# Optimization experiments

Measured on AMD Instinct MI355X. Metric: run time of the kernel, lower is better.

Reference implementation:

```python
import jax, jax.numpy as jnp
import numpy as np

B = 8192          # batch
CIN = 256         # in_channels
COUT = 64         # out_channels
K = 3             # kernel_size
NK = 4            # num_kernels
HIDDEN = int(CIN * 0.25)   # attention hidden = int(in_channels*ratio) = 64
TEMP = 34.0       # attention temperature
KAN_IN = 64 * 4   # base*4 = flattened conv output (COUT*2*2)
GRID_SIZE, SPLINE_ORDER = 5, 3
GMIN, GMAX = -1.0, 1.0
NUM_BASES = GRID_SIZE + SPLINE_ORDER  # 8


def setup_inputs() -> dict:
    key = jax.random.key(0)
    ks = jax.random.split(key, 8)
    s = 0.05
    return {
        "x": jax.random.normal(ks[0], (B, CIN, 4, 4), jnp.float32),
        # dynamic-conv kernel bank [num_kernels, out, in, k, k]
        "weight": jax.random.normal(ks[1], (NK, COUT, CIN, K, K), jnp.float32) * s,
        "bias": jnp.zeros((NK, COUT), jnp.float32),
        # Attention2D: GAP -> fc1 (1x1 conv == linear) -> ReLU -> fc2 -> softmax(/T)
        "fc1_w": jax.random.normal(ks[2], (HIDDEN, CIN), jnp.float32) * s,
        "fc1_b": jnp.zeros((HIDDEN,), jnp.float32),
        "fc2_w": jax.random.normal(ks[3], (NK, HIDDEN), jnp.float32) * s,
        "fc2_b": jnp.zeros((NK,), jnp.float32),
        # KANLinear params (efficient-KAN style)
        "kan_base_w": jax.random.normal(ks[4], (COUT, KAN_IN), jnp.float32) * s,
        "kan_spline_w": jax.random.normal(ks[5], (COUT, KAN_IN, NUM_BASES), jnp.float32) * s,
        "kan_spline_scaler": jnp.ones((COUT, KAN_IN), jnp.float32),
    }


def _bspline_bases(x):
    """Cox-de Boor B-spline bases; x [B, F] -> [B, F, GRID_SIZE+SPLINE_ORDER]."""
    h = (GMAX - GMIN) / GRID_SIZE
    # extended grid, shared across features: length grid_size + 2*order + 1 = 12
    grid = jnp.arange(-SPLINE_ORDER, GRID_SIZE + SPLINE_ORDER + 1, dtype=x.dtype) * h + GMIN
    xe = x[..., None]  # [B, F, 1]
    bases = ((xe >= grid[:-1]) & (xe < grid[1:])).astype(x.dtype)  # order 0
    for k in range(1, SPLINE_ORDER + 1):
        left = (xe - grid[: -(k + 1)]) / (grid[k:-1] - grid[: -(k + 1)]) * bases[..., :-1]
        right = (grid[k + 1:] - xe) / (grid[k + 1:] - grid[1:-k]) * bases[..., 1:]
        bases = left + right
    return bases  # [B, F, 8]


def reference(x, weight, bias, fc1_w, fc1_b, fc2_w, fc2_b,
              kan_base_w, kan_spline_w, kan_spline_scaler):
    b = x.shape[0]
    # --- Attention2D: softmax over kernel bank ---
    pooled = x.mean(axis=(2, 3))                                  # [B, CIN]
    hid = jax.nn.relu(pooled @ fc1_w.T + fc1_b)                   # [B, HIDDEN]
    attn = jax.nn.softmax((hid @ fc2_w.T + fc2_b) / TEMP, axis=-1)  # [B, NK]
    # --- per-sample dynamic conv, fused form ---
    # sum_k a[b,k] * conv(x, W_k) == conv with per-sample aggregated weight
    w_all = weight.reshape(NK * COUT, CIN, K, K)
    y = jax.lax.conv_general_dilated(
        x, w_all, window_strides=(1, 1), padding="VALID",
        dimension_numbers=("NCHW", "OIHW", "NCHW"))                # [B, NK*COUT, 2, 2]
    y = y.reshape(b, NK, COUT, y.shape[-2], y.shape[-1])
    conv_out = jnp.einsum("bk,bkohw->bohw", attn, y)
    conv_out = conv_out + (attn @ bias)[:, :, None, None]          # aggregated bias
    # --- KANLinear on flattened conv output ---
    feat = conv_out.reshape(b, -1)                                 # [B, 256]
    base_out = jax.nn.silu(feat) @ kan_base_w.T                    # [B, COUT]
    bases = _bspline_bases(feat)                                   # [B, 256, 8]
    spline_out = jnp.einsum("big,oig->bo", bases,
                            kan_spline_w * kan_spline_scaler[..., None])
    return base_out + spline_out                                   # [B, COUT]
```

## Files before the change

### kernel.cpp

```cpp
#include <hip/hip_runtime.h>

#define BT   8192
#define MS   16

typedef _Float16 half8  __attribute__((ext_vector_type(8)));
typedef _Float16 half4v __attribute__((ext_vector_type(4)));
typedef float    floatx4  __attribute__((ext_vector_type(4)));
typedef float    floatx16 __attribute__((ext_vector_type(16)));

__global__ __launch_bounds__(256) void w3_transform(
    const float* __restrict__ weight, _Float16* __restrict__ W3)
{
    const int n = blockIdx.x;
    const int c = threadIdx.x;
    const float* src = weight + ((size_t)n * 256 + c) * 9;
    const int cc = c >> 5, ci = c & 31;
    #pragma unroll
    for (int ij = 0; ij < 9; ++ij) {
        W3[((size_t)(cc * 9 + ij) * 256 + n) * 32 + ci] = (_Float16)src[ij];
    }
}

__global__ __launch_bounds__(256) void wk3_transform(
    const float* __restrict__ base_w, const float* __restrict__ spline_w,
    const float* __restrict__ scaler, const float* __restrict__ fc1_w,
    _Float16* __restrict__ Wk3, _Float16* __restrict__ Wf3)
{
    const int st = blockIdx.x;
    const int tid = threadIdx.x;
    if (st < 72) {
        #pragma unroll
        for (int u = 0; u < 8; ++u) {
            const int idx = u * 256 + tid;
            const int n = idx >> 5, kk = idx & 31;
            const int k = st * 32 + kk;
            float v;
            if (k < 256) {
                v = base_w[n * 256 + k];
            } else {
                const int r = k - 256;
                const int i = r >> 3, g = r & 7;
                v = spline_w[((size_t)n * 256 + i) * 8 + g] * scaler[n * 256 + i];
            }
            Wk3[(size_t)st * 2048 + idx] = (_Float16)v;
        }
    } else {
        const int st2 = st - 72;
        #pragma unroll
        for (int u = 0; u < 8; ++u) {
            const int idx = u * 256 + tid;
            const int n = idx >> 5, kk = idx & 31;
            Wf3[(size_t)st2 * 2048 + idx] = (_Float16)fc1_w[n * 256 + st2 * 32 + kk];
        }
    }
}

__device__ __forceinline__ void bases8(float xv, _Float16* dst) {
    float g[12];
    #pragma unroll
    for (int u = 0; u < 12; ++u) g[u] = (float)(u - 3) * 0.4f - 1.0f;
    float dt[12];
    #pragma unroll
    for (int u = 0; u < 12; ++u) dt[u] = xv - g[u];
    float t0[11];
    #pragma unroll
    for (int t = 0; t < 11; ++t)
        t0[t] = (xv >= g[t] && xv < g[t + 1]) ? 1.f : 0.f;
    float t1[10];
    #pragma unroll
    for (int t = 0; t < 10; ++t)
        t1[t] = dt[t] * (1.0f / (g[t + 1] - g[t])) * t0[t]
              - dt[t + 2] * (1.0f / (g[t + 2] - g[t + 1])) * t0[t + 1];
    float t2[9];
    #pragma unroll
    for (int t = 0; t < 9; ++t)
        t2[t] = dt[t] * (1.0f / (g[t + 2] - g[t])) * t1[t]
              - dt[t + 3] * (1.0f / (g[t + 3] - g[t + 1])) * t1[t + 1];
    half8 hb;
    #pragma unroll
    for (int t = 0; t < 8; ++t) {
        float b = dt[t] * (1.0f / (g[t + 3] - g[t])) * t2[t]
                - dt[t + 4] * (1.0f / (g[t + 4] - g[t + 1])) * t2[t + 1];
        hb[t] = (_Float16)b;
    }
    *(half8*)dst = hb;
}

__global__ __launch_bounds__(512, 4) void fused_kernel(
    const float* __restrict__ x, const _Float16* __restrict__ W3,
    const _Float16* __restrict__ Wk3, const _Float16* __restrict__ Wf3,
    const float* __restrict__ bias, const float* __restrict__ fc1_b,
    const float* __restrict__ fc2_w, const float* __restrict__ fc2_b,
    float* __restrict__ out)
{
    __shared__ __align__(16) char smem[16 * 2312 * 2];
    __shared__ float hid_lds[16 * 68];
    __shared__ float attn_s[16][4];

    _Float16* Xs  = (_Float16*)smem;
    _Float16* Pl  = (_Float16*)(smem + 20992);
    _Float16* Act = (_Float16*)smem;

    const int tid = threadIdx.x;
    const int wv = tid >> 6, lane = tid & 63;
    const int nl = lane & 15, q = lane >> 4;
    const int cg = wv & 3, rh = wv >> 2;
    const int b0 = blockIdx.x * MS;

    const int posr = nl & 3;
    const int aLane = (nl >> 2) * 656 + ((posr >> 1) * 4 + (posr & 1)) * 40 + q * 8;
    int lbW[4];
    #pragma unroll
    for (int kb = 0; kb < 4; ++kb) lbW[kb] = ((cg + 4 * kb) * 16 + nl) * 32 + q * 8;

    const int s_ = tid >> 5, cch = tid & 31;
    const float* xg = x + ((size_t)(b0 + s_) * 256 + cch) * 16;
    _Float16* xd = &Xs[s_ * 656 + cch];

    floatx4 acc[2][4];
    #pragma unroll
    for (int rr = 0; rr < 2; ++rr)
        #pragma unroll
        for (int kb = 0; kb < 4; ++kb) acc[rr][kb] = floatx4{0.f, 0.f, 0.f, 0.f};

    floatx16 r = *(const floatx16*)xg;

    for (int cc = 0; cc < 8; ++cc) {
        __syncthreads();
        #pragma unroll
        for (int p = 0; p < 16; ++p) xd[p * 40] = (_Float16)r[p];
        {
            float sm = 0.f;
            #pragma unroll
            for (int p = 0; p < 16; ++p) sm += r[p];
            Pl[s_ * 264 + cc * 32 + cch] = (_Float16)(sm * (1.0f / 16.0f));
        }
        if (cc < 7) r = *(const floatx16*)(xg + (cc + 1) * 512);
        __syncthreads();

        #pragma unroll 3
        for (int ij = 0; ij < 9; ++ij) {
            const int step = cc * 9 + ij;
            const int p0 = (ij / 3) * 4 + (ij % 3);
            const _Float16* wstep = W3 + (size_t)step * 8192;
            half8 bF[4];
            #pragma unroll
            for (int kb = 0; kb < 4; ++kb) bF[kb] = *(const half8*)(wstep + lbW[kb]);
            half8 aF[2];
            #pragma unroll
            for (int rr = 0; rr < 2; ++rr)
                aF[rr] = *(const half8*)&Xs[(rh * 2 + rr) * 2624 + aLane + p0 * 40];
            #pragma unroll
            for (int rr = 0; rr < 2; ++rr)
                #pragma unroll
                for (int kb = 0; kb < 4; ++kb)
                    acc[rr][kb] = __builtin_amdgcn_mfma_f32_16x16x32_f16(aF[rr], bF[kb], acc[rr][kb], 0, 0, 0);
        }
    }

    if (rh == 0) {
        floatx4 a1 = floatx4{0.f, 0.f, 0.f, 0.f};
        const _Float16* wfb = Wf3 + ((cg * 16 + nl) * 32 + q * 8);
        const _Float16* pb = &Pl[nl * 264 + q * 8];
        #pragma unroll
        for (int st = 0; st < 8; ++st) {
            const half8 aF = *(const half8*)(pb + st * 32);
            const half8 bF = *(const half8*)(wfb + st * 2048);
            a1 = __builtin_amdgcn_mfma_f32_16x16x32_f16(aF, bF, a1, 0, 0, 0);
        }
        const int h = cg * 16 + nl;
        const float fb = fc1_b[h];
        #pragma unroll
        for (int reg = 0; reg < 4; ++reg)
            hid_lds[(q * 4 + reg) * 68 + h] = fmaxf(a1[reg] + fb, 0.f);
    }
    __syncthreads();

    if (wv == 0) {
        const int s = lane >> 2, kb = lane & 3;
        float l = fc2_b[kb];
        #pragma unroll 8
        for (int h = 0; h < 64; ++h) l += hid_lds[s * 68 + h] * fc2_w[kb * 64 + h];
        float m = fmaxf(l, __shfl_xor(l, 1));
        m = fmaxf(m, __shfl_xor(m, 2));
        const float e = __expf((l - m) * (1.0f / 34.0f));
        float sm = e + __shfl_xor(e, 1);
        sm += __shfl_xor(sm, 2);
        attn_s[s][kb] = e / sm;
    }
    __syncthreads();

    {
        const int o = cg * 16 + nl;
        const float bb0 = bias[o], bb1 = bias[64 + o], bb2 = bias[128 + o], bb3 = bias[192 + o];
        #pragma unroll
        for (int rr = 0; rr < 2; ++rr) {
            const int s = (rh * 2 + rr) * 4 + q;
            const float a0 = attn_s[s][0], a1 = attn_s[s][1], a2 = attn_s[s][2], a3 = attn_s[s][3];
            const float badd = a0 * bb0 + a1 * bb1 + a2 * bb2 + a3 * bb3;
            float f[4];
            #pragma unroll
            for (int e = 0; e < 4; ++e)
                f[e] = a0 * acc[rr][0][e] + a1 * acc[rr][1][e]
                     + a2 * acc[rr][2][e] + a3 * acc[rr][3][e] + badd;
            half4v sv;
            #pragma unroll
            for (int e = 0; e < 4; ++e) {
                const float ex = __expf(-f[e]);
                sv[e] = (_Float16)(f[e] * __builtin_amdgcn_rcpf(1.f + ex));
            }
            *(half4v*)&Act[s * 2312 + o * 4] = sv;
            #pragma unroll
            for (int e = 0; e < 4; ++e)
                bases8(f[e], &Act[s * 2312 + 256 + (o * 4 + e) * 8]);
        }
    }
    __syncthreads();

    {
        floatx4 a2 = floatx4{0.f, 0.f, 0.f, 0.f};
        const _Float16* wkb = Wk3 + ((size_t)(cg * 16 + nl) * 32 + q * 8);
        const _Float16* ab = &Act[nl * 2312 + q * 8];
        #pragma unroll 6
        for (int i = 0; i < 36; ++i) {
            const int st = rh * 36 + i;
            const half8 aF = *(const half8*)(ab + st * 32);
            const half8 bF = *(const half8*)(wkb + (size_t)st * 2048);
            a2 = __builtin_amdgcn_mfma_f32_16x16x32_f16(aF, bF, a2, 0, 0, 0);
        }
        if (rh == 1) *(floatx4*)&hid_lds[cg * 256 + lane * 4] = a2;
        __syncthreads();
        if (rh == 0) {
            const floatx4 p = *(const floatx4*)&hid_lds[cg * 256 + lane * 4];
            a2 = a2 + p;
            #pragma unroll
            for (int reg = 0; reg < 4; ++reg)
                out[(size_t)(b0 + q * 4 + reg) * 64 + cg * 16 + nl] = a2[reg];
        }
    }
}

extern "C" void kernel_launch(void* const* d_in, const int* in_sizes, int n_in,
                              void* d_out, int out_size, void* d_ws, size_t ws_size,
                              hipStream_t stream) {
    const float* x          = (const float*)d_in[0];
    const float* weight     = (const float*)d_in[1];
    const float* bias       = (const float*)d_in[2];
    const float* fc1_w      = (const float*)d_in[3];
    const float* fc1_b      = (const float*)d_in[4];
    const float* fc2_w      = (const float*)d_in[5];
    const float* fc2_b      = (const float*)d_in[6];
    const float* kan_base_w = (const float*)d_in[7];
    const float* kan_spline = (const float*)d_in[8];
    const float* kan_scaler = (const float*)d_in[9];
    float* out = (float*)d_out;

    _Float16* W3  = (_Float16*)d_ws;
    _Float16* Wk3 = W3 + (size_t)72 * 8192;
    _Float16* Wf3 = Wk3 + (size_t)72 * 2048;

    w3_transform<<<256, 256, 0, stream>>>(weight, W3);
    wk3_transform<<<80, 256, 0, stream>>>(kan_base_w, kan_spline, kan_scaler,
                                          fc1_w, Wk3, Wf3);
    fused_kernel<<<BT / MS, 512, 0, stream>>>(x, W3, Wk3, Wf3, bias, fc1_b,
                                              fc2_w, fc2_b, out);
}
```

Measured before the change: 276.6 us.

## Shrink tile to 8 samples, double-buffer x in LDS, prefetch weight fragments

The fused kernel now handles 8 samples per block with 256 threads instead of 16 with 512, so there are twice as many blocks and each wave covers all sample rows. The x staging buffer is double-buffered so the next channel chunk is written to LDS while the current one is consumed, which removes one barrier per chunk. Weight fragments for the conv and KAN MFMAs are software-prefetched one step ahead. The trade-off is that the MFMA M dimension (16) is now only half used in the attention and KAN stages, and every block re-reads the full weight set, doubling global weight traffic per sample.

```diff
diff --git a/kernel.cpp b/kernel.cpp
--- a/kernel.cpp
+++ b/kernel.cpp
@@ -1,7 +1,8 @@
 #include <hip/hip_runtime.h>
 
 #define BT   8192
-#define MS   16
+#define MS   8
+#define XBUF (MS * 656)
 
 typedef _Float16 half8  __attribute__((ext_vector_type(8)));
 typedef _Float16 half4v __attribute__((ext_vector_type(4)));
@@ -86,25 +87,25 @@
     *(half8*)dst = hb;
 }
 
-__global__ __launch_bounds__(512, 4) void fused_kernel(
+__global__ __launch_bounds__(256, 4) void fused_kernel(
     const float* __restrict__ x, const _Float16* __restrict__ W3,
     const _Float16* __restrict__ Wk3, const _Float16* __restrict__ Wf3,
     const float* __restrict__ bias, const float* __restrict__ fc1_b,
     const float* __restrict__ fc2_w, const float* __restrict__ fc2_b,
     float* __restrict__ out)
 {
-    __shared__ __align__(16) char smem[16 * 2312 * 2];
-    __shared__ float hid_lds[16 * 68];
-    __shared__ float attn_s[16][4];
+    __shared__ __align__(16) char smem[MS * 2312 * 2];
+    __shared__ float hid_lds[MS * 68];
+    __shared__ float attn_s[MS][4];
 
     _Float16* Xs  = (_Float16*)smem;
-    _Float16* Pl  = (_Float16*)(smem + 20992);
+    _Float16* Pl  = (_Float16*)(smem + 2 * XBUF * 2);
     _Float16* Act = (_Float16*)smem;
 
     const int tid = threadIdx.x;
     const int wv = tid >> 6, lane = tid & 63;
     const int nl = lane & 15, q = lane >> 4;
-    const int cg = wv & 3, rh = wv >> 2;
+    const int cg = wv;
     const int b0 = blockIdx.x * MS;
 
     const int posr = nl & 3;
@@ -115,78 +116,101 @@
 
     const int s_ = tid >> 5, cch = tid & 31;
     const float* xg = x + ((size_t)(b0 + s_) * 256 + cch) * 16;
-    _Float16* xd = &Xs[s_ * 656 + cch];
 
     floatx4 acc[2][4];
     #pragma unroll
-    for (int rr = 0; rr < 2; ++rr)
-        #pragma unroll
-        for (int kb = 0; kb < 4; ++kb) acc[rr][kb] = floatx4{0.f, 0.f, 0.f, 0.f};
+    for (int rt = 0; rt < 2; ++rt)
+        #pragma unroll
+        for (int kb = 0; kb < 4; ++kb) acc[rt][kb] = floatx4{0.f, 0.f, 0.f, 0.f};
 
     floatx16 r = *(const floatx16*)xg;
+    {
+        _Float16* xd = &Xs[s_ * 656 + cch];
+        #pragma unroll
+        for (int p = 0; p < 16; ++p) xd[p * 40] = (_Float16)r[p];
+        float sm = 0.f;
+        #pragma unroll
+        for (int p = 0; p < 16; ++p) sm += r[p];
+        Pl[s_ * 264 + cch] = (_Float16)(sm * (1.0f / 16.0f));
+    }
+    r = *(const floatx16*)(xg + 512);
+    __syncthreads();
 
     for (int cc = 0; cc < 8; ++cc) {
-        __syncthreads();
-        #pragma unroll
-        for (int p = 0; p < 16; ++p) xd[p * 40] = (_Float16)r[p];
-        {
+        const int cur = cc & 1;
+        if (cc < 7) {
+            _Float16* xd = &Xs[(cur ^ 1) * XBUF + s_ * 656 + cch];
+            #pragma unroll
+            for (int p = 0; p < 16; ++p) xd[p * 40] = (_Float16)r[p];
             float sm = 0.f;
             #pragma unroll
             for (int p = 0; p < 16; ++p) sm += r[p];
-            Pl[s_ * 264 + cc * 32 + cch] = (_Float16)(sm * (1.0f / 16.0f));
-        }
-        if (cc < 7) r = *(const floatx16*)(xg + (cc + 1) * 512);
-        __syncthreads();
-
-        #pragma unroll 3
+            Pl[s_ * 264 + (cc + 1) * 32 + cch] = (_Float16)(sm * (1.0f / 16.0f));
+        }
+        if (cc < 6) r = *(const floatx16*)(xg + (cc + 2) * 512);
+
+        const _Float16* wst = W3 + (size_t)cc * 9 * 8192;
+        const _Float16* xb = &Xs[cur * XBUF + aLane];
+        half8 bFc[4];
+        #pragma unroll
+        for (int kb = 0; kb < 4; ++kb) bFc[kb] = *(const half8*)(wst + lbW[kb]);
+        #pragma unroll
         for (int ij = 0; ij < 9; ++ij) {
-            const int step = cc * 9 + ij;
-            const int p0 = (ij / 3) * 4 + (ij % 3);
-            const _Float16* wstep = W3 + (size_t)step * 8192;
-            half8 bF[4];
-            #pragma unroll
-            for (int kb = 0; kb < 4; ++kb) bF[kb] = *(const half8*)(wstep + lbW[kb]);
-            half8 aF[2];
-            #pragma unroll
-            for (int rr = 0; rr < 2; ++rr)
-                aF[rr] = *(const half8*)&Xs[(rh * 2 + rr) * 2624 + aLane + p0 * 40];
-            #pragma unroll
-            for (int rr = 0; rr < 2; ++rr)
+            half8 bFn[4];
+            if (ij < 8) {
                 #pragma unroll
                 for (int kb = 0; kb < 4; ++kb)
-                    acc[rr][kb] = __builtin_amdgcn_mfma_f32_16x16x32_f16(aF[rr], bF[kb], acc[rr][kb], 0, 0, 0);
-        }
-    }
-
-    if (rh == 0) {
+                    bFn[kb] = *(const half8*)(wst + (ij + 1) * 8192 + lbW[kb]);
+            }
+            const int p0 = (ij / 3) * 4 + (ij % 3);
+            half8 aF[2];
+            #pragma unroll
+            for (int rt = 0; rt < 2; ++rt)
+                aF[rt] = *(const half8*)&xb[rt * 2624 + p0 * 40];
+            #pragma unroll
+            for (int rt = 0; rt < 2; ++rt)
+                #pragma unroll
+                for (int kb = 0; kb < 4; ++kb)
+                    acc[rt][kb] = __builtin_amdgcn_mfma_f32_16x16x32_f16(aF[rt], bFc[kb], acc[rt][kb], 0, 0, 0);
+            #pragma unroll
+            for (int kb = 0; kb < 4; ++kb) bFc[kb] = bFn[kb];
+        }
+        __syncthreads();
+    }
+
+    {
         floatx4 a1 = floatx4{0.f, 0.f, 0.f, 0.f};
         const _Float16* wfb = Wf3 + ((cg * 16 + nl) * 32 + q * 8);
-        const _Float16* pb = &Pl[nl * 264 + q * 8];
+        const _Float16* pb = &Pl[(nl & 7) * 264 + q * 8];
         #pragma unroll
         for (int st = 0; st < 8; ++st) {
             const half8 aF = *(const half8*)(pb + st * 32);
             const half8 bF = *(const half8*)(wfb + st * 2048);
             a1 = __builtin_amdgcn_mfma_f32_16x16x32_f16(aF, bF, a1, 0, 0, 0);
         }
-        const int h = cg * 16 + nl;
-        const float fb = fc1_b[h];
-        #pragma unroll
-        for (int reg = 0; reg < 4; ++reg)
-            hid_lds[(q * 4 + reg) * 68 + h] = fmaxf(a1[reg] + fb, 0.f);
+        if (q < 2) {
+            const int h = cg * 16 + nl;
+            const float fb = fc1_b[h];
+            #pragma unroll
+            for (int reg = 0; reg < 4; ++reg)
+                hid_lds[(q * 4 + reg) * 68 + h] = fmaxf(a1[reg] + fb, 0.f);
+        }
     }
     __syncthreads();
 
     if (wv == 0) {
         const int s = lane >> 2, kb = lane & 3;
-        float l = fc2_b[kb];
-        #pragma unroll 8
-        for (int h = 0; h < 64; ++h) l += hid_lds[s * 68 + h] * fc2_w[kb * 64 + h];
-        float m = fmaxf(l, __shfl_xor(l, 1));
-        m = fmaxf(m, __shfl_xor(m, 2));
-        const float e = __expf((l - m) * (1.0f / 34.0f));
-        float sm = e + __shfl_xor(e, 1);
-        sm += __shfl_xor(sm, 2);
-        attn_s[s][kb] = e / sm;
+        if (s < 8) {
+            float l = fc2_b[kb];
+            #pragma unroll 8
+            for (int h = 0; h < 64; ++h) l += hid_lds[s * 68 + h] * fc2_w[kb * 64 + h];
+            float m = fmaxf(l, __shfl_xor(l, 1));
+            m = fmaxf(m, __shfl_xor(m, 2));
+            const float e = __expf((l - m) * (1.0f / 34.0f));
+            float sm = e + __shfl_xor(e, 1);
+            sm += __shfl_xor(sm, 2);
+            attn_s[s][kb] = e / sm;
+        }
     }
     __syncthreads();
 
@@ -194,15 +218,15 @@
         const int o = cg * 16 + nl;
         const float bb0 = bias[o], bb1 = bias[64 + o], bb2 = bias[128 + o], bb3 = bias[192 + o];
         #pragma unroll
-        for (int rr = 0; rr < 2; ++rr) {
-            const int s = (rh * 2 + rr) * 4 + q;
+        for (int rt = 0; rt < 2; ++rt) {
+            const int s = rt * 4 + q;
             const float a0 = attn_s[s][0], a1 = attn_s[s][1], a2 = attn_s[s][2], a3 = attn_s[s][3];
             const float badd = a0 * bb0 + a1 * bb1 + a2 * bb2 + a3 * bb3;
             float f[4];
             #pragma unroll
             for (int e = 0; e < 4; ++e)
-                f[e] = a0 * acc[rr][0][e] + a1 * acc[rr][1][e]
-                     + a2 * acc[rr][2][e] + a3 * acc[rr][3][e] + badd;
+                f[e] = a0 * acc[rt][0][e] + a1 * acc[rt][1][e]
+                     + a2 * acc[rt][2][e] + a3 * acc[rt][3][e] + badd;
             half4v sv;
             #pragma unroll
             for (int e = 0; e < 4; ++e) {
@@ -220,19 +244,17 @@
     {
         floatx4 a2 = floatx4{0.f, 0.f, 0.f, 0.f};
         const _Float16* wkb = Wk3 + ((size_t)(cg * 16 + nl) * 32 + q * 8);
-        const _Float16* ab = &Act[nl * 2312 + q * 8];
-        #pragma unroll 6
-        for (int i = 0; i < 36; ++i) {
-            const int st = rh * 36 + i;
+        const _Float16* ab = &Act[(nl & 7) * 2312 + q * 8];
+        half8 bFc = *(const half8*)(wkb);
+        #pragma unroll 8
+        for (int st = 0; st < 72; ++st) {
+            half8 bFn;
+            if (st < 71) bFn = *(const half8*)(wkb + (size_t)(st + 1) * 2048);
             const half8 aF = *(const half8*)(ab + st * 32);
-            const half8 bF = *(const half8*)(wkb + (size_t)st * 2048);
-            a2 = __builtin_amdgcn_mfma_f32_16x16x32_f16(aF, bF, a2, 0, 0, 0);
-        }
-        if (rh == 1) *(floatx4*)&hid_lds[cg * 256 + lane * 4] = a2;
-        __syncthreads();
-        if (rh == 0) {
-            const floatx4 p = *(const floatx4*)&hid_lds[cg * 256 + lane * 4];
-            a2 = a2 + p;
+            a2 = __builtin_amdgcn_mfma_f32_16x16x32_f16(aF, bFc, a2, 0, 0, 0);
+            bFc = bFn;
+        }
+        if (q < 2) {
             #pragma unroll
             for (int reg = 0; reg < 4; ++reg)
                 out[(size_t)(b0 + q * 4 + reg) * 64 + cg * 16 + nl] = a2[reg];
@@ -262,6 +284,6 @@
     w3_transform<<<256, 256, 0, stream>>>(weight, W3);
     wk3_transform<<<80, 256, 0, stream>>>(kan_base_w, kan_spline, kan_scaler,
                                           fc1_w, Wk3, Wf3);
-    fused_kernel<<<BT / MS, 512, 0, stream>>>(x, W3, Wk3, Wf3, bias, fc1_b,
+    fused_kernel<<<BT / MS, 256, 0, stream>>>(x, W3, Wk3, Wf3, bias, fc1_b,
                                               fc2_w, fc2_b, out);
 }
```

New measurement: 283.7 us. 2.6% more time.

## Double-buffer conv input, split MFMA by kernel-bank, closed-form B-spline bases

Applied to the files above, without the earlier changes.

The conv phase now double-buffers the staged x tile in LDS, so the next channel chunk is written while MFMAs run on the current one, which drops one barrier per chunk. Weight fragments are prefetched two steps ahead in registers. Work is re-split so each wave covers all 4 sample row-tiles but only 2 of the 4 kernel-bank columns, with the partial attention-weighted sums reduced through LDS. The Cox-de Boor recursion is replaced by a closed-form uniform cubic B-spline evaluation, and the KAN MFMA loop also prefetches weights. The costs are higher register pressure and an extra LDS reduction step.

```diff
diff --git a/kernel.cpp b/kernel.cpp
--- a/kernel.cpp
+++ b/kernel.cpp
@@ -2,6 +2,7 @@
 
 #define BT   8192
 #define MS   16
+#define XBUF (MS * 656)
 
 typedef _Float16 half8  __attribute__((ext_vector_type(8)));
 typedef _Float16 half4v __attribute__((ext_vector_type(4)));
@@ -55,33 +56,26 @@
     }
 }
 
-__device__ __forceinline__ void bases8(float xv, _Float16* dst) {
-    float g[12];
-    #pragma unroll
-    for (int u = 0; u < 12; ++u) g[u] = (float)(u - 3) * 0.4f - 1.0f;
-    float dt[12];
-    #pragma unroll
-    for (int u = 0; u < 12; ++u) dt[u] = xv - g[u];
-    float t0[11];
-    #pragma unroll
-    for (int t = 0; t < 11; ++t)
-        t0[t] = (xv >= g[t] && xv < g[t + 1]) ? 1.f : 0.f;
-    float t1[10];
-    #pragma unroll
-    for (int t = 0; t < 10; ++t)
-        t1[t] = dt[t] * (1.0f / (g[t + 1] - g[t])) * t0[t]
-              - dt[t + 2] * (1.0f / (g[t + 2] - g[t + 1])) * t0[t + 1];
-    float t2[9];
-    #pragma unroll
-    for (int t = 0; t < 9; ++t)
-        t2[t] = dt[t] * (1.0f / (g[t + 2] - g[t])) * t1[t]
-              - dt[t + 3] * (1.0f / (g[t + 3] - g[t + 1])) * t1[t + 1];
+__device__ __forceinline__ void bases8c(float xv, _Float16* dst) {
+    const float t = (xv + 2.2f) * 2.5f;
+    const float ft = floorf(t);
+    const int idx = (int)ft;
+    const float u = t - ft, v = 1.f - u;
+    const float u2 = u * u, v2 = v * v;
+    const float c3 = u2 * u * (1.f / 6.f);
+    const float c2 = (1.f / 6.f) + 0.5f * (u + u2 - u2 * u);
+    const float c1 = (1.f / 6.f) + 0.5f * (v + v2 - v2 * v);
+    const float c0 = v2 * v * (1.f / 6.f);
     half8 hb;
     #pragma unroll
-    for (int t = 0; t < 8; ++t) {
-        float b = dt[t] * (1.0f / (g[t + 3] - g[t])) * t2[t]
-                - dt[t + 4] * (1.0f / (g[t + 4] - g[t + 1])) * t2[t + 1];
-        hb[t] = (_Float16)b;
+    for (int tt = 0; tt < 8; ++tt) {
+        const int d = idx - tt;
+        float b = 0.f;
+        b = (d == 0) ? c3 : b;
+        b = (d == 1) ? c2 : b;
+        b = (d == 2) ? c1 : b;
+        b = (d == 3) ? c0 : b;
+        hb[tt] = (_Float16)b;
     }
     *(half8*)dst = hb;
 }
@@ -93,12 +87,12 @@
     const float* __restrict__ fc2_w, const float* __restrict__ fc2_b,
     float* __restrict__ out)
 {
-    __shared__ __align__(16) char smem[16 * 2312 * 2];
-    __shared__ float hid_lds[16 * 68];
-    __shared__ float attn_s[16][4];
+    __shared__ __align__(16) char smem[MS * 2312 * 2];
+    __shared__ float hid_lds[MS * 68];
+    __shared__ float attn_s[MS][4];
 
     _Float16* Xs  = (_Float16*)smem;
-    _Float16* Pl  = (_Float16*)(smem + 20992);
+    _Float16* Pl  = (_Float16*)(smem + 2 * XBUF * 2);
     _Float16* Act = (_Float16*)smem;
 
     const int tid = threadIdx.x;
@@ -109,53 +103,72 @@
 
     const int posr = nl & 3;
     const int aLane = (nl >> 2) * 656 + ((posr >> 1) * 4 + (posr & 1)) * 40 + q * 8;
-    int lbW[4];
-    #pragma unroll
-    for (int kb = 0; kb < 4; ++kb) lbW[kb] = ((cg + 4 * kb) * 16 + nl) * 32 + q * 8;
+    const int lbW0 = (((rh * 2 + 0) * 4 + cg) * 16 + nl) * 32 + q * 8;
+    const int lbW1 = (((rh * 2 + 1) * 4 + cg) * 16 + nl) * 32 + q * 8;
 
     const int s_ = tid >> 5, cch = tid & 31;
     const float* xg = x + ((size_t)(b0 + s_) * 256 + cch) * 16;
-    _Float16* xd = &Xs[s_ * 656 + cch];
-
-    floatx4 acc[2][4];
+
+    floatx4 acc[4][2];
     #pragma unroll
-    for (int rr = 0; rr < 2; ++rr)
-        #pragma unroll
-        for (int kb = 0; kb < 4; ++kb) acc[rr][kb] = floatx4{0.f, 0.f, 0.f, 0.f};
+    for (int rt = 0; rt < 4; ++rt) {
+        acc[rt][0] = floatx4{0.f, 0.f, 0.f, 0.f};
+        acc[rt][1] = floatx4{0.f, 0.f, 0.f, 0.f};
+    }
 
     floatx16 r = *(const floatx16*)xg;
-
+    {
+        _Float16* xd = &Xs[s_ * 656 + cch];
+        #pragma unroll
+        for (int p = 0; p < 16; ++p) xd[p * 40] = (_Float16)r[p];
+        float sm = 0.f;
+        #pragma unroll
+        for (int p = 0; p < 16; ++p) sm += r[p];
+        Pl[s_ * 264 + cch] = (_Float16)(sm * (1.0f / 16.0f));
+    }
+    r = *(const floatx16*)(xg + 512);
+    __syncthreads();
+
+    #pragma unroll 1
     for (int cc = 0; cc < 8; ++cc) {
+        const int cur = cc & 1;
+        if (cc < 7) {
+            _Float16* xd = &Xs[(cur ^ 1) * XBUF + s_ * 656 + cch];
+            #pragma unroll
+            for (int p = 0; p < 16; ++p) xd[p * 40] = (_Float16)r[p];
+            float sm = 0.f;
+            #pragma unroll
+            for (int p = 0; p < 16; ++p) sm += r[p];
+            Pl[s_ * 264 + (cc + 1) * 32 + cch] = (_Float16)(sm * (1.0f / 16.0f));
+        }
+        if (cc < 6) r = *(const floatx16*)(xg + (cc + 2) * 512);
+
+        const _Float16* wst = W3 + (size_t)cc * 9 * 8192;
+        const _Float16* xb = &Xs[cur * XBUF + aLane];
+        half8 bA0 = *(const half8*)(wst + lbW0);
+        half8 bB0 = *(const half8*)(wst + lbW1);
+        half8 bA1 = *(const half8*)(wst + 8192 + lbW0);
+        half8 bB1 = *(const half8*)(wst + 8192 + lbW1);
+        #pragma unroll
+        for (int ij = 0; ij < 9; ++ij) {
+            half8 bA2, bB2;
+            if (ij < 7) {
+                bA2 = *(const half8*)(wst + (ij + 2) * 8192 + lbW0);
+                bB2 = *(const half8*)(wst + (ij + 2) * 8192 + lbW1);
+            }
+            const int p0 = (ij / 3) * 4 + (ij % 3);
+            half8 aF[4];
+            #pragma unroll
+            for (int rt = 0; rt < 4; ++rt)
+                aF[rt] = *(const half8*)&xb[rt * 2624 + p0 * 40];
+            #pragma unroll
+            for (int rt = 0; rt < 4; ++rt) {
+                acc[rt][0] = __builtin_amdgcn_mfma_f32_16x16x32_f16(aF[rt], bA0, acc[rt][0], 0, 0, 0);
+                acc[rt][1] = __builtin_amdgcn_mfma_f32_16x16x32_f16(aF[rt], bB0, acc[rt][1], 0, 0, 0);
+            }
+            bA0 = bA1; bB0 = bB1; bA1 = bA2; bB1 = bB2;
+        }
         __syncthreads();
-        #pragma unroll
-        for (int p = 0; p < 16; ++p) xd[p * 40] = (_Float16)r[p];
-        {
-            float sm = 0.f;
-            #pragma unroll
-            for (int p = 0; p < 16; ++p) sm += r[p];
-            Pl[s_ * 264 + cc * 32 + cch] = (_Float16)(sm * (1.0f / 16.0f));
-        }
-        if (cc < 7) r = *(const floatx16*)(xg + (cc + 1) * 512);
-        __syncthreads();
-
-        #pragma unroll 3
-        for (int ij = 0; ij < 9; ++ij) {
-            const int step = cc * 9 + ij;
-            const int p0 = (ij / 3) * 4 + (ij % 3);
-            const _Float16* wstep = W3 + (size_t)step * 8192;
-            half8 bF[4];
-            #pragma unroll
-            for (int kb = 0; kb < 4; ++kb) bF[kb] = *(const half8*)(wstep + lbW[kb]);
-            half8 aF[2];
-            #pragma unroll
-            for (int rr = 0; rr < 2; ++rr)
-                aF[rr] = *(const half8*)&Xs[(rh * 2 + rr) * 2624 + aLane + p0 * 40];
-            #pragma unroll
-            for (int rr = 0; rr < 2; ++rr)
-                #pragma unroll
-                for (int kb = 0; kb < 4; ++kb)
-                    acc[rr][kb] = __builtin_amdgcn_mfma_f32_16x16x32_f16(aF[rr], bF[kb], acc[rr][kb], 0, 0, 0);
-        }
     }
 
     if (rh == 0) {
@@ -190,19 +203,35 @@
     }
     __syncthreads();
 
-    {
-        const int o = cg * 16 + nl;
+    const int o = cg * 16 + nl;
+    if (rh == 1) {
+        #pragma unroll
+        for (int rt = 0; rt < 4; ++rt) {
+            const int s = rt * 4 + q;
+            const float a2w = attn_s[s][2], a3w = attn_s[s][3];
+            #pragma unroll
+            for (int e = 0; e < 4; ++e) {
+                float* slot = (float*)&Act[s * 2312 + 256 + (o * 4 + e) * 8];
+                slot[0] = a2w * acc[rt][0][e] + a3w * acc[rt][1][e];
+            }
+        }
+    }
+    __syncthreads();
+
+    if (rh == 0) {
         const float bb0 = bias[o], bb1 = bias[64 + o], bb2 = bias[128 + o], bb3 = bias[192 + o];
         #pragma unroll
-        for (int rr = 0; rr < 2; ++rr) {
-            const int s = (rh * 2 + rr) * 4 + q;
-            const float a0 = attn_s[s][0], a1 = attn_s[s][1], a2 = attn_s[s][2], a3 = attn_s[s][3];
+        for (int rt = 0; rt < 4; ++rt) {
+            const int s = rt * 4 + q;
+            const float a0 = attn_s[s][0], a1 = attn_s[s][1],
+                        a2 = attn_s[s][2], a3 = attn_s[s][3];
             const float badd = a0 * bb0 + a1 * bb1 + a2 * bb2 + a3 * bb3;
             float f[4];
             #pragma unroll
-            for (int e = 0; e < 4; ++e)
-                f[e] = a0 * acc[rr][0][e] + a1 * acc[rr][1][e]
-                     + a2 * acc[rr][2][e] + a3 * acc[rr][3][e] + badd;
+            for (int e = 0; e < 4; ++e) {
+                const float part = ((float*)&Act[s * 2312 + 256 + (o * 4 + e) * 8])[0];
+                f[e] = a0 * acc[rt][0][e] + a1 * acc[rt][1][e] + part + badd;
+            }
             half4v sv;
             #pragma unroll
             for (int e = 0; e < 4; ++e) {
@@ -212,7 +241,7 @@
             *(half4v*)&Act[s * 2312 + o * 4] = sv;
             #pragma unroll
             for (int e = 0; e < 4; ++e)
-                bases8(f[e], &Act[s * 2312 + 256 + (o * 4 + e) * 8]);
+                bases8c(f[e], &Act[s * 2312 + 256 + (o * 4 + e) * 8]);
         }
     }
     __syncthreads();
@@ -221,12 +250,16 @@
         floatx4 a2 = floatx4{0.f, 0.f, 0.f, 0.f};
         const _Float16* wkb = Wk3 + ((size_t)(cg * 16 + nl) * 32 + q * 8);
         const _Float16* ab = &Act[nl * 2312 + q * 8];
-        #pragma unroll 6
+        const int st0 = rh * 36;
+        half8 kb0 = *(const half8*)(wkb + (size_t)st0 * 2048);
+        half8 kb1 = *(const half8*)(wkb + (size_t)(st0 + 1) * 2048);
+        #pragma unroll 4
         for (int i = 0; i < 36; ++i) {
-            const int st = rh * 36 + i;
-            const half8 aF = *(const half8*)(ab + st * 32);
-            const half8 bF = *(const half8*)(wkb + (size_t)st * 2048);
-            a2 = __builtin_amdgcn_mfma_f32_16x16x32_f16(aF, bF, a2, 0, 0, 0);
+            half8 kb2;
+            if (i < 34) kb2 = *(const half8*)(wkb + (size_t)(st0 + i + 2) * 2048);
+            const half8 aF = *(const half8*)(ab + (st0 + i) * 32);
+            a2 = __builtin_amdgcn_mfma_f32_16x16x32_f16(aF, kb0, a2, 0, 0, 0);
+            kb0 = kb1; kb1 = kb2;
         }
         if (rh == 1) *(floatx4*)&hid_lds[cg * 256 + lane * 4] = a2;
         __syncthreads();
```

New measurement: 250.5 us. 1.1x faster.
